# Kernel tuning notes

Hardware: AMD Instinct MI355X
Metric: run time of the kernel (lower is better)

Reference implementation:

```python
import jax, jax.numpy as jnp
import numpy as np

B, S, H, NH, HD = 4, 4096, 1024, 16, 64

def setup_inputs() -> dict:
    key = jax.random.key(0)
    ks = jax.random.split(key, 5)
    scale = 1.0 / np.sqrt(H)
    return {
        "hidden_states": jax.random.normal(ks[0], (B, S, H), dtype=jnp.float32),
        "Wq": jax.random.normal(ks[1], (H, H), dtype=jnp.float32) * scale,
        "Wk": jax.random.normal(ks[2], (H, H), dtype=jnp.float32) * scale,
        "Wv": jax.random.normal(ks[3], (H, H), dtype=jnp.float32) * scale,
        "Wo": jax.random.normal(ks[4], (H, H), dtype=jnp.float32) * scale,
    }

def reference(hidden_states, Wq, Wk, Wv, Wo):
    b, s, h = hidden_states.shape
    # torch nn.Linear: y = x @ W.T
    q = (hidden_states @ Wq.T).reshape(b, s, NH, HD)
    k = (hidden_states @ Wk.T).reshape(b, s, NH, HD)
    v = (hidden_states @ Wv.T).reshape(b, s, NH, HD)
    # feature map: ELU (as in source, no +1)
    q = jax.nn.elu(q)
    k = jax.nn.elu(k)
    # per-head kv state: sum over sequence of outer products k_s v_s^T -> [b,h,d,e]
    kv = jnp.einsum('bshd,bshe->bhde', k, v)
    out = jnp.einsum('bqhd,bhde->bqhe', q, kv)  # [b,s,h,e]
    out = out.reshape(b, s, h)
    return out @ Wo.T  # dropout p=0.0 is identity
```

## Files before the change

### kernel.cpp

```cpp
#include <hip/hip_runtime.h>
#include <cstdint>
#include <cstddef>

#define B_  4
#define S_  4096
#define H_  1024
#define NH_ 16
#define HD_ 64
#define M_  (B_*S_)

typedef __bf16 bf16x8 __attribute__((ext_vector_type(8)));
typedef float  f32x4  __attribute__((ext_vector_type(4)));

__device__ __forceinline__ unsigned short f2b(float f) {
  union { float f; unsigned u; } v; v.f = f;
  unsigned r = v.u + 0x7FFFu + ((v.u >> 16) & 1u);
  return (unsigned short)(r >> 16);
}
__device__ __forceinline__ float b2f(unsigned short u) {
  union { unsigned u; float f; } v; v.u = ((unsigned)u) << 16;
  return v.f;
}

#define GLD16(g, l) __builtin_amdgcn_global_load_lds( \
    (const __attribute__((address_space(1))) void*)(g), \
    (__attribute__((address_space(3))) void*)(l), 16, 0, 0)

__global__ void cast_f32_bf16(const float* __restrict__ src,
                              unsigned short* __restrict__ dst, int n4) {
  int i = blockIdx.x * blockDim.x + threadIdx.x;
  if (i >= n4) return;
  float4 f = reinterpret_cast<const float4*>(src)[i];
  ushort4 o;
  o.x = f2b(f.x); o.y = f2b(f.y); o.z = f2b(f.z); o.w = f2b(f.w);
  reinterpret_cast<ushort4*>(dst)[i] = o;
}

template<int ACT, bool OUTBF>
__global__ __launch_bounds__(256, 2) void gemm_bt(
    const unsigned short* __restrict__ A,
    const unsigned short* __restrict__ Bt,
    void* __restrict__ Cv) {
  __shared__ __align__(16) unsigned short As[128 * 32];
  __shared__ __align__(16) unsigned short Bs[128 * 32];

  const int nwg = gridDim.x;
  const int nx  = nwg >> 3;
  const int bid = blockIdx.x;
  const int b2  = (bid & 7) * nx + (bid >> 3);
  const int tileM = (b2 >> 3) << 7;
  const int tileN = (b2 & 7) << 7;

  const int lane = threadIdx.x & 63;
  const int wv   = threadIdx.x >> 6;
  const int wm   = (wv >> 1) * 64;
  const int wn   = (wv & 1) * 64;
  const int fr   = lane & 15;
  const int fq   = lane >> 4;

  const int c0 = wv * 128 + lane;
  const int c1 = c0 + 64;
  const int r0 = c0 >> 2, k0 = (c0 & 3) * 8;
  const int r1 = c1 >> 2, k1 = (c1 & 3) * 8;

  f32x4 zero = {0.f, 0.f, 0.f, 0.f};
  f32x4 acc[4][4];
#pragma unroll
  for (int i = 0; i < 4; i++)
#pragma unroll
    for (int j = 0; j < 4; j++) acc[i][j] = zero;

  for (int kk = 0; kk < 1024; kk += 32) {
    GLD16(A  + (size_t)(tileM + r0) * 1024 + kk + k0, &As[wv * 1024]);
    GLD16(A  + (size_t)(tileM + r1) * 1024 + kk + k1, &As[wv * 1024 + 512]);
    GLD16(Bt + (size_t)(tileN + r0) * 1024 + kk + k0, &Bs[wv * 1024]);
    GLD16(Bt + (size_t)(tileN + r1) * 1024 + kk + k1, &Bs[wv * 1024 + 512]);
    __syncthreads();

    bf16x8 af[4], bfv[4];
#pragma unroll
    for (int i = 0; i < 4; i++)
      af[i] = *reinterpret_cast<const bf16x8*>(&As[(wm + i * 16 + fr) * 32 + fq * 8]);
#pragma unroll
    for (int j = 0; j < 4; j++)
      bfv[j] = *reinterpret_cast<const bf16x8*>(&Bs[(wn + j * 16 + fr) * 32 + fq * 8]);
#pragma unroll
    for (int i = 0; i < 4; i++)
#pragma unroll
      for (int j = 0; j < 4; j++)
        acc[i][j] = __builtin_amdgcn_mfma_f32_16x16x32_bf16(af[i], bfv[j], acc[i][j], 0, 0, 0);
    __syncthreads();
  }

#pragma unroll
  for (int i = 0; i < 4; i++)
#pragma unroll
    for (int j = 0; j < 4; j++)
#pragma unroll
      for (int r = 0; r < 4; r++) {
        int row = tileM + wm + i * 16 + fq * 4 + r;
        int col = tileN + wn + j * 16 + fr;
        float v = acc[i][j][r];
        if (ACT == 1) v = v > 0.f ? v : (expf(v) - 1.f);
        if (OUTBF)
          ((unsigned short*)Cv)[(size_t)row * 1024 + col] = f2b(v);
        else
          ((float*)Cv)[(size_t)row * 1024 + col] = v;
      }
}

__global__ __launch_bounds__(256) void kv_partial(
    const unsigned short* __restrict__ Kb,
    const unsigned short* __restrict__ Vb,
    float* __restrict__ kvp) {
  __shared__ __align__(16) unsigned short kt[32 * 64];
  __shared__ __align__(16) unsigned short vt[32 * 64];
  const int bh = blockIdx.x >> 3;
  const int ch = blockIdx.x & 7;
  const int b  = bh >> 4, h = bh & 15;
  const int t  = threadIdx.x;
  const int rr = t >> 3;
  const int cc = (t & 7) * 8;
  const int d0 = (t >> 4) * 4;
  const int e0 = (t & 15) * 4;

  float acc[4][4] = {};
  for (int s0 = ch * 512; s0 < ch * 512 + 512; s0 += 32) {
    size_t g = (size_t)(b * S_ + s0 + rr) * H_ + h * 64 + cc;
    *reinterpret_cast<uint4*>(&kt[rr * 64 + cc]) = *reinterpret_cast<const uint4*>(Kb + g);
    *reinterpret_cast<uint4*>(&vt[rr * 64 + cc]) = *reinterpret_cast<const uint4*>(Vb + g);
    __syncthreads();
#pragma unroll 4
    for (int ss = 0; ss < 32; ss++) {
      ushort4 k4 = *reinterpret_cast<const ushort4*>(&kt[ss * 64 + d0]);
      ushort4 v4 = *reinterpret_cast<const ushort4*>(&vt[ss * 64 + e0]);
      float kf[4] = {b2f(k4.x), b2f(k4.y), b2f(k4.z), b2f(k4.w)};
      float vf[4] = {b2f(v4.x), b2f(v4.y), b2f(v4.z), b2f(v4.w)};
#pragma unroll
      for (int i = 0; i < 4; i++)
#pragma unroll
        for (int j = 0; j < 4; j++) acc[i][j] += kf[i] * vf[j];
    }
    __syncthreads();
  }
  float* outp = kvp + (size_t)blockIdx.x * 4096;
#pragma unroll
  for (int i = 0; i < 4; i++)
#pragma unroll
    for (int j = 0; j < 4; j++) outp[(d0 + i) * 64 + e0 + j] = acc[i][j];
}

__global__ __launch_bounds__(256) void kv_reduce(
    const float* __restrict__ kvp, unsigned short* __restrict__ KVbT) {
  const int bh = blockIdx.x;
#pragma unroll
  for (int i = 0; i < 16; i++) {
    int idx = threadIdx.x + i * 256;
    float s = 0.f;
#pragma unroll
    for (int ch = 0; ch < 8; ch++) s += kvp[(size_t)(bh * 8 + ch) * 4096 + idx];
    int d = idx >> 6, e = idx & 63;
    KVbT[(size_t)bh * 4096 + e * 64 + d] = f2b(s);
  }
}

__global__ __launch_bounds__(64) void qkv_apply(
    const unsigned short* __restrict__ Qb,
    const unsigned short* __restrict__ KVbT,
    unsigned short* __restrict__ Ob) {
  const int blk = blockIdx.x;
  const int mt  = blk & 63;
  const int bh  = blk >> 6;
  const int b   = bh >> 4, h = bh & 15;
  const int lane = threadIdx.x;
  const int fr = lane & 15, fq = lane >> 4;
  const size_t rowbase = (size_t)b * S_ + mt * 64;

  f32x4 zero = {0.f, 0.f, 0.f, 0.f};
  f32x4 acc[4][4];
#pragma unroll
  for (int i = 0; i < 4; i++)
#pragma unroll
    for (int j = 0; j < 4; j++) acc[i][j] = zero;

#pragma unroll
  for (int kk = 0; kk < 64; kk += 32) {
    bf16x8 af[4], bfv[4];
#pragma unroll
    for (int i = 0; i < 4; i++)
      af[i] = *reinterpret_cast<const bf16x8*>(
          Qb + (rowbase + i * 16 + fr) * H_ + h * 64 + kk + fq * 8);
#pragma unroll
    for (int j = 0; j < 4; j++)
      bfv[j] = *reinterpret_cast<const bf16x8*>(
          KVbT + (size_t)bh * 4096 + (j * 16 + fr) * 64 + kk + fq * 8);
#pragma unroll
    for (int i = 0; i < 4; i++)
#pragma unroll
      for (int j = 0; j < 4; j++)
        acc[i][j] = __builtin_amdgcn_mfma_f32_16x16x32_bf16(af[i], bfv[j], acc[i][j], 0, 0, 0);
  }

#pragma unroll
  for (int i = 0; i < 4; i++)
#pragma unroll
    for (int j = 0; j < 4; j++)
#pragma unroll
      for (int r = 0; r < 4; r++)
        Ob[(rowbase + i * 16 + fq * 4 + r) * H_ + h * 64 + j * 16 + fr] =
            f2b(acc[i][j][r]);
}

extern "C" void kernel_launch(void* const* d_in, const int* in_sizes, int n_in,
                              void* d_out, int out_size, void* d_ws, size_t ws_size,
                              hipStream_t stream) {
  (void)in_sizes; (void)n_in; (void)out_size; (void)ws_size;
  const float* X  = (const float*)d_in[0];
  const float* Wq = (const float*)d_in[1];
  const float* Wk = (const float*)d_in[2];
  const float* Wv = (const float*)d_in[3];
  const float* Wo = (const float*)d_in[4];

  char*  ws  = (char*)d_ws;
  size_t off = 0;
  auto alloc = [&](size_t bytes) -> char* {
    char* p = ws + off;
    off += (bytes + 255) & ~(size_t)255;
    return p;
  };
  unsigned short* Xb   = (unsigned short*)alloc((size_t)M_ * H_ * 2);
  unsigned short* Wqb  = (unsigned short*)alloc((size_t)H_ * H_ * 2);
  unsigned short* Wkb  = (unsigned short*)alloc((size_t)H_ * H_ * 2);
  unsigned short* Wvb  = (unsigned short*)alloc((size_t)H_ * H_ * 2);
  unsigned short* Wob  = (unsigned short*)alloc((size_t)H_ * H_ * 2);
  unsigned short* Qb   = (unsigned short*)alloc((size_t)M_ * H_ * 2);
  unsigned short* Kb   = (unsigned short*)alloc((size_t)M_ * H_ * 2);
  unsigned short* Vb   = (unsigned short*)alloc((size_t)M_ * H_ * 2);
  float*          kvp  = (float*)alloc((size_t)64 * 8 * 4096 * 4);
  unsigned short* KVbT = (unsigned short*)alloc((size_t)64 * 4096 * 2);
  unsigned short* Ob   = Xb;

  cast_f32_bf16<<<(M_ * H_) / 1024, 256, 0, stream>>>(X, Xb, (M_ * H_) / 4);
  cast_f32_bf16<<<(H_ * H_) / 1024, 256, 0, stream>>>(Wq, Wqb, (H_ * H_) / 4);
  cast_f32_bf16<<<(H_ * H_) / 1024, 256, 0, stream>>>(Wk, Wkb, (H_ * H_) / 4);
  cast_f32_bf16<<<(H_ * H_) / 1024, 256, 0, stream>>>(Wv, Wvb, (H_ * H_) / 4);
  cast_f32_bf16<<<(H_ * H_) / 1024, 256, 0, stream>>>(Wo, Wob, (H_ * H_) / 4);

  gemm_bt<1, true><<<1024, 256, 0, stream>>>(Xb, Wqb, Qb);
  gemm_bt<1, true><<<1024, 256, 0, stream>>>(Xb, Wkb, Kb);
  gemm_bt<0, true><<<1024, 256, 0, stream>>>(Xb, Wvb, Vb);

  kv_partial<<<512, 256, 0, stream>>>(Kb, Vb, kvp);
  kv_reduce<<<64, 256, 0, stream>>>(kvp, KVbT);
  qkv_apply<<<4096, 64, 0, stream>>>(Qb, KVbT, Ob);

  gemm_bt<0, false><<<1024, 256, 0, stream>>>(Ob, Wob, (float*)d_out);
}
```

Before: 299.2 us.

## Fuse QKV GEMM, fold KV state into Wo, use pipelined 256-tile GEMM

```diff
diff --git a/kernel.cpp b/kernel.cpp
--- a/kernel.cpp
+++ b/kernel.cpp
@@ -6,7 +6,6 @@
 #define S_  4096
 #define H_  1024
 #define NH_ 16
-#define HD_ 64
 #define M_  (B_*S_)
 
 typedef __bf16 bf16x8 __attribute__((ext_vector_type(8)));
@@ -25,6 +24,10 @@
 #define GLD16(g, l) __builtin_amdgcn_global_load_lds( \
     (const __attribute__((address_space(1))) void*)(g), \
     (__attribute__((address_space(3))) void*)(l), 16, 0, 0)
+
+#define VM(n)  asm volatile("s_waitcnt vmcnt(" #n ")" ::: "memory")
+#define BAR()  do { asm volatile("" ::: "memory"); __builtin_amdgcn_s_barrier(); \
+                    asm volatile("" ::: "memory"); } while (0)
 
 __global__ void cast_f32_bf16(const float* __restrict__ src,
                               unsigned short* __restrict__ dst, int n4) {
@@ -36,77 +39,141 @@
   reinterpret_cast<ushort4*>(dst)[i] = o;
 }
 
-template<int ACT, bool OUTBF>
-__global__ __launch_bounds__(256, 2) void gemm_bt(
-    const unsigned short* __restrict__ A,
-    const unsigned short* __restrict__ Bt,
-    void* __restrict__ Cv) {
-  __shared__ __align__(16) unsigned short As[128 * 32];
-  __shared__ __align__(16) unsigned short Bs[128 * 32];
-
-  const int nwg = gridDim.x;
-  const int nx  = nwg >> 3;
-  const int bid = blockIdx.x;
-  const int b2  = (bid & 7) * nx + (bid >> 3);
-  const int tileM = (b2 >> 3) << 7;
-  const int tileN = (b2 & 7) << 7;
-
-  const int lane = threadIdx.x & 63;
-  const int wv   = threadIdx.x >> 6;
-  const int wm   = (wv >> 1) * 64;
-  const int wn   = (wv & 1) * 64;
-  const int fr   = lane & 15;
-  const int fq   = lane >> 4;
-
-  const int c0 = wv * 128 + lane;
-  const int c1 = c0 + 64;
-  const int r0 = c0 >> 2, k0 = (c0 & 3) * 8;
-  const int r1 = c1 >> 2, k1 = (c1 & 3) * 8;
+__global__ void cast_w4(const float* __restrict__ w0, const float* __restrict__ w1,
+                        const float* __restrict__ w2, const float* __restrict__ w3,
+                        unsigned short* __restrict__ dst) {
+  int i = blockIdx.x * blockDim.x + threadIdx.x;
+  int w = i >> 18, j = i & 0x3FFFF;
+  const float* src = (w == 0) ? w0 : (w == 1) ? w1 : (w == 2) ? w2 : w3;
+  float4 f = reinterpret_cast<const float4*>(src)[j];
+  ushort4 o;
+  o.x = f2b(f.x); o.y = f2b(f.y); o.z = f2b(f.z); o.w = f2b(f.w);
+  reinterpret_cast<ushort4*>(dst)[i] = o;
+}
+
+template<int MODE>
+__global__ __launch_bounds__(512, 2) void gemm256(
+    const unsigned short* __restrict__ A_,
+    const unsigned short* __restrict__ Bt_,
+    void* __restrict__ out) {
+  __shared__ __align__(16) unsigned short LDS[2][2][16384];
+
+  const int NTN = (MODE == 0) ? 12 : 4;
+  const int nx  = gridDim.x >> 3;
+  const int b2  = (blockIdx.x & 7) * nx + (blockIdx.x >> 3);
+  const int tileM = (b2 / NTN) << 8;
+  const int tileN = (b2 % NTN) << 8;
+
+  const unsigned short* Bt_e =
+      (MODE == 1) ? (Bt_ + ((size_t)(tileM >> 12) << 20)) : Bt_;
+
+  const int tid  = threadIdx.x;
+  const int lane = tid & 63, wv = tid >> 6;
+  const int wmi  = wv >> 2;
+  const int wni  = wv & 3;
+  const int fr   = lane & 15, fq = lane >> 4;
+
+  const int sr0 = tid >> 3,          sc0 = (tid & 7) ^ (sr0 & 7);
+  const int sr1 = (tid + 512) >> 3,  sc1 = (tid & 7) ^ (sr1 & 7);
+
+#define STG(NB, ARR, HM, SRC, RB, TT) do {                                      \
+    GLD16((SRC) + (size_t)((RB) + (HM)*128 + sr0) * 1024 + (TT)*64 + sc0*8,     \
+          &LDS[NB][ARR][(HM)*8192 + wv*512]);                                   \
+    GLD16((SRC) + (size_t)((RB) + (HM)*128 + sr1) * 1024 + (TT)*64 + sc1*8,     \
+          &LDS[NB][ARR][(HM)*8192 + 4096 + wv*512]);                            \
+  } while (0)
 
   f32x4 zero = {0.f, 0.f, 0.f, 0.f};
-  f32x4 acc[4][4];
-#pragma unroll
-  for (int i = 0; i < 4; i++)
-#pragma unroll
-    for (int j = 0; j < 4; j++) acc[i][j] = zero;
-
-  for (int kk = 0; kk < 1024; kk += 32) {
-    GLD16(A  + (size_t)(tileM + r0) * 1024 + kk + k0, &As[wv * 1024]);
-    GLD16(A  + (size_t)(tileM + r1) * 1024 + kk + k1, &As[wv * 1024 + 512]);
-    GLD16(Bt + (size_t)(tileN + r0) * 1024 + kk + k0, &Bs[wv * 1024]);
-    GLD16(Bt + (size_t)(tileN + r1) * 1024 + kk + k1, &Bs[wv * 1024 + 512]);
-    __syncthreads();
-
-    bf16x8 af[4], bfv[4];
-#pragma unroll
-    for (int i = 0; i < 4; i++)
-      af[i] = *reinterpret_cast<const bf16x8*>(&As[(wm + i * 16 + fr) * 32 + fq * 8]);
-#pragma unroll
-    for (int j = 0; j < 4; j++)
-      bfv[j] = *reinterpret_cast<const bf16x8*>(&Bs[(wn + j * 16 + fr) * 32 + fq * 8]);
-#pragma unroll
-    for (int i = 0; i < 4; i++)
-#pragma unroll
-      for (int j = 0; j < 4; j++)
-        acc[i][j] = __builtin_amdgcn_mfma_f32_16x16x32_bf16(af[i], bfv[j], acc[i][j], 0, 0, 0);
-    __syncthreads();
+  f32x4 acc[2][2][4][2];
+#pragma unroll
+  for (int a = 0; a < 2; a++)
+#pragma unroll
+    for (int b = 0; b < 2; b++)
+#pragma unroll
+      for (int m = 0; m < 4; m++)
+#pragma unroll
+        for (int n = 0; n < 2; n++) acc[a][b][m][n] = zero;
+
+#define PHASE(CB, MQ, NQ, ...) do {                                             \
+    bf16x8 af[4][2], bv[2][2];                                                  \
+    _Pragma("unroll")                                                           \
+    for (int m = 0; m < 4; m++) {                                               \
+      int r = (MQ)*128 + wmi*64 + m*16 + fr;                                    \
+      af[m][0] = *(const bf16x8*)&LDS[CB][0][r*64 + (( fq   ) ^ (r&7))*8];      \
+      af[m][1] = *(const bf16x8*)&LDS[CB][0][r*64 + ((4+fq  ) ^ (r&7))*8];      \
+    }                                                                           \
+    _Pragma("unroll")                                                           \
+    for (int n = 0; n < 2; n++) {                                               \
+      int r = (NQ)*128 + wni*32 + n*16 + fr;                                    \
+      bv[n][0] = *(const bf16x8*)&LDS[CB][1][r*64 + (( fq   ) ^ (r&7))*8];      \
+      bv[n][1] = *(const bf16x8*)&LDS[CB][1][r*64 + ((4+fq  ) ^ (r&7))*8];      \
+    }                                                                           \
+    __VA_ARGS__;                                                                \
+    __builtin_amdgcn_s_setprio(1);                                              \
+    _Pragma("unroll")                                                           \
+    for (int m = 0; m < 4; m++)                                                 \
+      _Pragma("unroll")                                                         \
+      for (int n = 0; n < 2; n++) {                                             \
+        acc[MQ][NQ][m][n] = __builtin_amdgcn_mfma_f32_16x16x32_bf16(            \
+            af[m][0], bv[n][0], acc[MQ][NQ][m][n], 0, 0, 0);                    \
+        acc[MQ][NQ][m][n] = __builtin_amdgcn_mfma_f32_16x16x32_bf16(            \
+            af[m][1], bv[n][1], acc[MQ][NQ][m][n], 0, 0, 0);                    \
+      }                                                                         \
+    __builtin_amdgcn_s_setprio(0);                                              \
+  } while (0)
+
+  STG(0, 0, 0, A_,   tileM, 0);
+  STG(0, 0, 1, A_,   tileM, 0);
+  STG(0, 1, 0, Bt_e, tileN, 0);
+  STG(0, 1, 1, Bt_e, tileN, 0);
+  VM(0);
+  BAR();
+
+  int cb = 0;
+  for (int t = 0; t < 15; ++t) {
+    const int nb = cb ^ 1;
+    PHASE(cb, 0, 0, STG(nb, 0, 0, A_, tileM, t + 1);
+                    STG(nb, 1, 0, Bt_e, tileN, t + 1));
+    VM(6); BAR();
+    PHASE(cb, 0, 1, STG(nb, 1, 1, Bt_e, tileN, t + 1));
+    VM(6); BAR();
+    PHASE(cb, 1, 0, STG(nb, 0, 1, A_, tileM, t + 1));
+    BAR();
+    PHASE(cb, 1, 1, );
+    VM(4); BAR();
+    cb = nb;
   }
-
-#pragma unroll
-  for (int i = 0; i < 4; i++)
-#pragma unroll
-    for (int j = 0; j < 4; j++)
-#pragma unroll
-      for (int r = 0; r < 4; r++) {
-        int row = tileM + wm + i * 16 + fq * 4 + r;
-        int col = tileN + wn + j * 16 + fr;
-        float v = acc[i][j][r];
-        if (ACT == 1) v = v > 0.f ? v : (expf(v) - 1.f);
-        if (OUTBF)
-          ((unsigned short*)Cv)[(size_t)row * 1024 + col] = f2b(v);
-        else
-          ((float*)Cv)[(size_t)row * 1024 + col] = v;
-      }
+  PHASE(cb, 0, 0, );
+  VM(2); BAR();
+  PHASE(cb, 0, 1, );
+  VM(0); BAR();
+  PHASE(cb, 1, 0, );
+  PHASE(cb, 1, 1, );
+
+#pragma unroll
+  for (int mq = 0; mq < 2; mq++)
+#pragma unroll
+    for (int nq = 0; nq < 2; nq++)
+#pragma unroll
+      for (int m = 0; m < 4; m++)
+#pragma unroll
+        for (int n = 0; n < 2; n++)
+#pragma unroll
+          for (int r = 0; r < 4; r++) {
+            int row = tileM + mq * 128 + wmi * 64 + m * 16 + fq * 4 + r;
+            int col = tileN + nq * 128 + wni * 32 + n * 16 + fr;
+            float v = acc[mq][nq][m][n][r];
+            if (MODE == 0) {
+              int reg = col >> 10, lc = col & 1023;
+              if (reg < 2) v = v > 0.f ? v : (expf(v) - 1.f);
+              ((unsigned short*)out)[(size_t)reg * ((size_t)M_ * H_) +
+                                     (size_t)row * H_ + lc] = f2b(v);
+            } else {
+              ((float*)out)[(size_t)row * H_ + col] = v;
+            }
+          }
+#undef PHASE
+#undef STG
 }
 
 __global__ __launch_bounds__(256) void kv_partial(
@@ -151,7 +218,7 @@
 }
 
 __global__ __launch_bounds__(256) void kv_reduce(
-    const float* __restrict__ kvp, unsigned short* __restrict__ KVbT) {
+    const float* __restrict__ kvp, unsigned short* __restrict__ KVb) {
   const int bh = blockIdx.x;
 #pragma unroll
   for (int i = 0; i < 16; i++) {
@@ -159,22 +226,20 @@
     float s = 0.f;
 #pragma unroll
     for (int ch = 0; ch < 8; ch++) s += kvp[(size_t)(bh * 8 + ch) * 4096 + idx];
-    int d = idx >> 6, e = idx & 63;
-    KVbT[(size_t)bh * 4096 + e * 64 + d] = f2b(s);
+    KVb[(size_t)bh * 4096 + idx] = f2b(s);
   }
 }
 
-__global__ __launch_bounds__(64) void qkv_apply(
-    const unsigned short* __restrict__ Qb,
-    const unsigned short* __restrict__ KVbT,
-    unsigned short* __restrict__ Ob) {
-  const int blk = blockIdx.x;
-  const int mt  = blk & 63;
-  const int bh  = blk >> 6;
-  const int b   = bh >> 4, h = bh & 15;
-  const int lane = threadIdx.x;
+__global__ __launch_bounds__(256) void merge_m(
+    const unsigned short* __restrict__ KVb,
+    const unsigned short* __restrict__ Wob,
+    unsigned short* __restrict__ MbT) {
+  const int bh = blockIdx.x >> 2;
+  const int nc = blockIdx.x & 3;
+  const int b  = bh >> 4, h = bh & 15;
+  const int lane = threadIdx.x & 63, wv = threadIdx.x >> 6;
   const int fr = lane & 15, fq = lane >> 4;
-  const size_t rowbase = (size_t)b * S_ + mt * 64;
+  const int ncb = nc * 256 + wv * 64;
 
   f32x4 zero = {0.f, 0.f, 0.f, 0.f};
   f32x4 acc[4][4];
@@ -184,31 +249,30 @@
     for (int j = 0; j < 4; j++) acc[i][j] = zero;
 
 #pragma unroll
-  for (int kk = 0; kk < 64; kk += 32) {
-    bf16x8 af[4], bfv[4];
+  for (int kk = 0; kk < 2; kk++) {
+    bf16x8 af[4], bv[4];
 #pragma unroll
     for (int i = 0; i < 4; i++)
-      af[i] = *reinterpret_cast<const bf16x8*>(
-          Qb + (rowbase + i * 16 + fr) * H_ + h * 64 + kk + fq * 8);
+      af[i] = *(const bf16x8*)&KVb[(size_t)bh * 4096 + (i * 16 + fr) * 64 + kk * 32 + fq * 8];
 #pragma unroll
     for (int j = 0; j < 4; j++)
-      bfv[j] = *reinterpret_cast<const bf16x8*>(
-          KVbT + (size_t)bh * 4096 + (j * 16 + fr) * 64 + kk + fq * 8);
+      bv[j] = *(const bf16x8*)&Wob[(size_t)(ncb + j * 16 + fr) * 1024 + h * 64 + kk * 32 + fq * 8];
 #pragma unroll
     for (int i = 0; i < 4; i++)
 #pragma unroll
       for (int j = 0; j < 4; j++)
-        acc[i][j] = __builtin_amdgcn_mfma_f32_16x16x32_bf16(af[i], bfv[j], acc[i][j], 0, 0, 0);
+        acc[i][j] = __builtin_amdgcn_mfma_f32_16x16x32_bf16(af[i], bv[j], acc[i][j], 0, 0, 0);
   }
-
 #pragma unroll
   for (int i = 0; i < 4; i++)
 #pragma unroll
     for (int j = 0; j < 4; j++)
 #pragma unroll
-      for (int r = 0; r < 4; r++)
-        Ob[(rowbase + i * 16 + fq * 4 + r) * H_ + h * 64 + j * 16 + fr] =
-            f2b(acc[i][j][r]);
+      for (int r = 0; r < 4; r++) {
+        int n = ncb + j * 16 + fr;
+        int k = h * 64 + i * 16 + fq * 4 + r;
+        MbT[((size_t)b << 20) + (size_t)n * 1024 + k] = f2b(acc[i][j][r]);
+      }
 }
 
 extern "C" void kernel_launch(void* const* d_in, const int* in_sizes, int n_in,
@@ -229,30 +293,25 @@
     return p;
   };
   unsigned short* Xb   = (unsigned short*)alloc((size_t)M_ * H_ * 2);
-  unsigned short* Wqb  = (unsigned short*)alloc((size_t)H_ * H_ * 2);
-  unsigned short* Wkb  = (unsigned short*)alloc((size_t)H_ * H_ * 2);
-  unsigned short* Wvb  = (unsigned short*)alloc((size_t)H_ * H_ * 2);
-  unsigned short* Wob  = (unsigned short*)alloc((size_t)H_ * H_ * 2);
-  unsigned short* Qb   = (unsigned short*)alloc((size_t)M_ * H_ * 2);
-  unsigned short* Kb   = (unsigned short*)alloc((size_t)M_ * H_ * 2);
-  unsigned short* Vb   = (unsigned short*)alloc((size_t)M_ * H_ * 2);
+  unsigned short* Wcat = (unsigned short*)alloc((size_t)4 * H_ * H_ * 2);
+  unsigned short* QKVb = (unsigned short*)alloc((size_t)3 * M_ * H_ * 2);
   float*          kvp  = (float*)alloc((size_t)64 * 8 * 4096 * 4);
-  unsigned short* KVbT = (unsigned short*)alloc((size_t)64 * 4096 * 2);
-  unsigned short* Ob   = Xb;
+  unsigned short* KVb  = (unsigned short*)alloc((size_t)64 * 4096 * 2);
+  unsigned short* MbT  = (unsigned short*)alloc((size_t)4 * H_ * H_ * 2);
+
+  unsigned short* Qb = QKVb;
+  unsigned short* Kb = QKVb + (size_t)M_ * H_;
+  unsigned short* Vb = QKVb + (size_t)2 * M_ * H_;
+  unsigned short* Wob = Wcat + (size_t)3 * H_ * H_;
 
   cast_f32_bf16<<<(M_ * H_) / 1024, 256, 0, stream>>>(X, Xb, (M_ * H_) / 4);
-  cast_f32_bf16<<<(H_ * H_) / 1024, 256, 0, stream>>>(Wq, Wqb, (H_ * H_) / 4);
-  cast_f32_bf16<<<(H_ * H_) / 1024, 256, 0, stream>>>(Wk, Wkb, (H_ * H_) / 4);
-  cast_f32_bf16<<<(H_ * H_) / 1024, 256, 0, stream>>>(Wv, Wvb, (H_ * H_) / 4);
-  cast_f32_bf16<<<(H_ * H_) / 1024, 256, 0, stream>>>(Wo, Wob, (H_ * H_) / 4);
-
-  gemm_bt<1, true><<<1024, 256, 0, stream>>>(Xb, Wqb, Qb);
-  gemm_bt<1, true><<<1024, 256, 0, stream>>>(Xb, Wkb, Kb);
-  gemm_bt<0, true><<<1024, 256, 0, stream>>>(Xb, Wvb, Vb);
+  cast_w4<<<(4 * H_ * H_) / 1024, 256, 0, stream>>>(Wq, Wk, Wv, Wo, Wcat);
+
+  gemm256<0><<<768, 512, 0, stream>>>(Xb, Wcat, QKVb);
 
   kv_partial<<<512, 256, 0, stream>>>(Kb, Vb, kvp);
-  kv_reduce<<<64, 256, 0, stream>>>(kvp, KVbT);
-  qkv_apply<<<4096, 64, 0, stream>>>(Qb, KVbT, Ob);
-
-  gemm_bt<0, false><<<1024, 256, 0, stream>>>(Ob, Wob, (float*)d_out);
-}
+  kv_reduce<<<64, 256, 0, stream>>>(kvp, KVb);
+  merge_m<<<256, 256, 0, stream>>>(KVb, Wob, MbT);
+
+  gemm256<1><<<256, 512, 0, stream>>>(Qb, MbT, (float*)d_out);
+}
```

After: 258.1 us. -13.7%, faster.
